# Kernel optimization log

Measured on AMD Instinct MI355X. Metric: run time of the kernel, lower is better.

The kernel has to match this reference:

```python
import jax, jax.numpy as jnp
import numpy as np

N = 2048            # num nodes
AVG_DEG = 16
E0 = N * AVG_DEG    # random edges; self-loops appended -> E = E0 + N
IN_FEATS = 256
H = 16              # num_heads
HS = 32             # hidden_size (forced by linear001 = Linear(32,16))
D = HS // H         # head_dim = 2
EPS = 1e-5


def gat_conv(x, src, dst, W, al, ar, b):
    # DGL-style GATConv: x [N,F] -> [N,H,D]
    feat = (x @ W).reshape(N, H, D)                      # [N,H,D]
    el = (feat * al[None]).sum(-1)                       # [N,H] (src term)
    er = (feat * ar[None]).sum(-1)                       # [N,H] (dst term)
    e = jax.nn.leaky_relu(el[src] + er[dst], 0.2)        # [E,H]
    m = jax.ops.segment_max(e, dst, num_segments=N)      # segment softmax over incoming edges
    ex = jnp.exp(e - m[dst])
    s = jax.ops.segment_sum(ex, dst, num_segments=N)
    alpha = ex / s[dst]                                  # [E,H]
    out = jax.ops.segment_sum(alpha[:, :, None] * feat[src], dst, num_segments=N)
    return out + b.reshape(1, H, D)


def setup_inputs() -> dict:
    key = jax.random.key(0)
    ks = jax.random.split(key, 40)
    rn = lambda k, s, sc=0.1: (jax.random.normal(k, s, jnp.float32) * sc)
    loops = jnp.arange(N, dtype=jnp.int32)
    src = jnp.concatenate([jax.random.randint(ks[0], (E0,), 0, N, jnp.int32), loops])
    dst = jnp.concatenate([jax.random.randint(ks[1], (E0,), 0, N, jnp.int32), loops])
    inp = {
        'features': jax.random.normal(ks[2], (N, IN_FEATS), jnp.float32),
        'src': src, 'dst': dst,
        # GATConv 1
        'W1': rn(ks[3], (IN_FEATS, HS)), 'al1': rn(ks[4], (H, D)), 'ar1': rn(ks[5], (H, D)), 'bg1': rn(ks[6], (HS,)),
        # GATConv 2
        'W2': rn(ks[7], (HS, HS)), 'al2': rn(ks[8], (H, D)), 'ar2': rn(ks[9], (H, D)), 'bg2': rn(ks[10], (HS,)),
        # dense MHA projections
        'qw': rn(ks[11], (HS, HS)), 'qb': rn(ks[12], (HS,)),
        'kw': rn(ks[13], (HS, HS)), 'kb': rn(ks[14], (HS,)),
        'vw': rn(ks[15], (HS, HS)), 'vb': rn(ks[16], (HS,)),
        'ow': rn(ks[17], (HS, HS)), 'ob': rn(ks[18], (HS,)),
        # batchnorm affine
        'bn_g': jnp.ones((HS,), jnp.float32), 'bn_b': jnp.zeros((HS,), jnp.float32),
        # mlp
        'm1w': rn(ks[19], (HS, HS // 2)), 'm1b': rn(ks[20], (HS // 2,)),
        'm2w': rn(ks[21], (HS // 2, HS)), 'm2b': rn(ks[22], (HS,)),
        # scoring head
        'w001': rn(ks[23], (32, 16)), 'b001': rn(ks[24], (16,)),
        'w01': rn(ks[25], (16, 8)), 'b01': rn(ks[26], (8,)),
        'w1': rn(ks[27], (8, 4)), 'b1': rn(ks[28], (4,)),
        'w2': rn(ks[29], (4, 1)), 'b2': rn(ks[30], (1,)),
    }
    return inp


def reference(features, src, dst, W1, al1, ar1, bg1, W2, al2, ar2, bg2,
              qw, qb, kw, kb, vw, vb, ow, ob, bn_g, bn_b,
              m1w, m1b, m2w, m2b, w001, b001, w01, b01, w1, b1, w2, b2):
    h = gat_conv(features, src, dst, W1, al1, ar1, bg1).reshape(N, HS)
    h = gat_conv(h, src, dst, W2, al2, ar2, bg2).reshape(N, HS)
    # manual dense multi-head attention across all nodes
    Q = (h @ qw + qb).reshape(N, H, D)
    K = (h @ kw + kb).reshape(N, H, D)
    V = (h @ vw + vb).reshape(N, H, D)
    scores = jnp.einsum('nhd,mhd->hnm', Q, K) / jnp.sqrt(jnp.float32(D))  # [H,N,N]
    attn = jax.nn.softmax(scores, axis=-1)
    ao = jnp.einsum('hnm,mhd->nhd', attn, V).reshape(N, HS)
    ao = ao @ ow + ob
    # BatchNorm1d (training mode: batch stats, biased variance)
    mu = ao.mean(0)
    var = ao.var(0)
    ao = (ao - mu) / jnp.sqrt(var + EPS) * bn_g + bn_b
    # MLP
    ao = jax.nn.relu(ao @ m1w + m1b)
    ao = jax.nn.relu(ao @ m2w + m2b)
    # scoring head
    z = jax.nn.leaky_relu(ao @ w001 + b001, 0.01)
    z = jax.nn.leaky_relu(z @ w01 + b01, 0.01)
    z = jax.nn.leaky_relu(z @ w1 + b1, 0.01)
    return jax.nn.sigmoid(z @ w2 + b2)  # [N,1]
```

## Files before the change

### kernel.cpp

```cpp
#include <hip/hip_runtime.h>
#include <math.h>

#define NN 2048
#define NH 16
#define HSZ 32
#define INF_ 256
#define CAP 64

__global__ void __launch_bounds__(256) k_front(
    const float* __restrict__ x, const float* __restrict__ W1,
    const float* __restrict__ al, const float* __restrict__ ar,
    const int* __restrict__ src, const int* __restrict__ dst, int E,
    unsigned int* __restrict__ cnt, int* __restrict__ adj,
    const unsigned int* __restrict__ poisonRef, float* __restrict__ feat,
    float* __restrict__ el, float* __restrict__ er) {
    __shared__ float xs[4][INF_];
    __shared__ float row[4][HSZ];
    const int tid = threadIdx.x;
    const int gtid = blockIdx.x * 256 + tid;
    const int lane = tid & 63, wsl = tid >> 6, gw = gtid >> 6;
    const int j = lane & 31, half = lane >> 5;

    if (gtid < E) {
        unsigned int P = *poisonRef;
        int d = dst[gtid];
        unsigned int old = atomicAdd(&cnt[d], 1u);
        unsigned int pos = old - P;
        if (pos < CAP) adj[d * CAP + pos] = src[gtid];
    }

    int n = gw;
    ((float4*)xs[wsl])[lane] = ((const float4*)(x + (size_t)n * INF_))[lane];
    __syncthreads();
    float acc = 0.f;
    const float4* x4 = (const float4*)xs[wsl];
#pragma unroll
    for (int k4 = 0; k4 < 32; ++k4) {
        float4 xq = x4[half * 32 + k4];
        int k = half * 128 + 4 * k4;
        acc += xq.x * W1[(k + 0) * HSZ + j];
        acc += xq.y * W1[(k + 1) * HSZ + j];
        acc += xq.z * W1[(k + 2) * HSZ + j];
        acc += xq.w * W1[(k + 3) * HSZ + j];
    }
    acc += __shfl_xor(acc, 32);
    if (half == 0) {
        feat[n * HSZ + j] = acc;
        row[wsl][j] = acc;
    }
    __syncthreads();
    if (lane < NH) {
        el[n * NH + lane] =
            row[wsl][2 * lane] * al[2 * lane] + row[wsl][2 * lane + 1] * al[2 * lane + 1];
    } else if (lane < 2 * NH) {
        int h = lane - NH;
        er[n * NH + h] =
            row[wsl][2 * h] * ar[2 * h] + row[wsl][2 * h + 1] * ar[2 * h + 1];
    }
}

__global__ void __launch_bounds__(256) k_seg_gat2(
    const unsigned int* __restrict__ cnt, const int* __restrict__ adj,
    const unsigned int* __restrict__ poisonRef,
    const float* __restrict__ el, const float* __restrict__ er,
    const float* __restrict__ feat, const float* __restrict__ bg,
    const float* __restrict__ W2, const float* __restrict__ al2,
    const float* __restrict__ ar2, float* __restrict__ feat2,
    float* __restrict__ el2, float* __restrict__ er2) {
    __shared__ float row[4][HSZ];
    __shared__ float xv[4][HSZ];
    const int tid = threadIdx.x;
    const int gtid = blockIdx.x * 256 + tid;
    const int lane = tid & 63, wsl = tid >> 6, gw = gtid >> 6;
    const int j = lane & 31, half = lane >> 5;
    int n = gw;
    int h = lane >> 2, q = lane & 3;
    unsigned int deg = cnt[n] - *poisonRef;
    if (deg > CAP) deg = CAP;
    int base = n * CAP;
    float erv = er[n * NH + h];
    float sum = 0.f, a0 = 0.f, a1 = 0.f;
    for (unsigned int jj = q; jj < deg; jj += 4) {
        int s = adj[base + jj];
        float v = el[s * NH + h] + erv;
        v = v > 0.f ? v : 0.2f * v;
        float ex = __expf(v);
        float2 f = ((const float2*)feat)[s * NH + h];
        sum += ex; a0 += ex * f.x; a1 += ex * f.y;
    }
    sum += __shfl_xor(sum, 1); a0 += __shfl_xor(a0, 1); a1 += __shfl_xor(a1, 1);
    sum += __shfl_xor(sum, 2); a0 += __shfl_xor(a0, 2); a1 += __shfl_xor(a1, 2);
    if (q == 0) {
        float rs = 1.f / sum;
        row[wsl][2 * h]     = a0 * rs + bg[2 * h];
        row[wsl][2 * h + 1] = a1 * rs + bg[2 * h + 1];
    }
    __syncthreads();
    float acc = 0.f;
#pragma unroll
    for (int c = half * 16; c < half * 16 + 16; ++c) acc += row[wsl][c] * W2[c * HSZ + j];
    acc += __shfl_xor(acc, 32);
    if (half == 0) {
        feat2[n * HSZ + j] = acc;
        xv[wsl][j] = acc;
    }
    __syncthreads();
    if (lane < NH) {
        el2[n * NH + lane] =
            xv[wsl][2 * lane] * al2[2 * lane] + xv[wsl][2 * lane + 1] * al2[2 * lane + 1];
    } else if (lane < 2 * NH) {
        int h2 = lane - NH;
        er2[n * NH + h2] =
            xv[wsl][2 * h2] * ar2[2 * h2] + xv[wsl][2 * h2 + 1] * ar2[2 * h2 + 1];
    }
}

__global__ void __launch_bounds__(256) k_seg_qkv(
    const unsigned int* __restrict__ cnt, const int* __restrict__ adj,
    const unsigned int* __restrict__ poisonRef,
    const float* __restrict__ el2, const float* __restrict__ er2,
    const float* __restrict__ feat2, const float* __restrict__ bg,
    const float* __restrict__ qw, const float* __restrict__ qb,
    const float* __restrict__ kw, const float* __restrict__ kb,
    const float* __restrict__ vw, const float* __restrict__ vb,
    float* __restrict__ Q, float* __restrict__ KV) {
    __shared__ float row[4][HSZ];
    const int tid = threadIdx.x;
    const int gtid = blockIdx.x * 256 + tid;
    const int lane = tid & 63, wsl = tid >> 6, gw = gtid >> 6;
    const int j = lane & 31, half = lane >> 5;
    int n = gw;
    int h = lane >> 2, q = lane & 3;
    unsigned int deg = cnt[n] - *poisonRef;
    if (deg > CAP) deg = CAP;
    int base = n * CAP;
    float erv = er2[n * NH + h];
    float sum = 0.f, a0 = 0.f, a1 = 0.f;
    for (unsigned int jj = q; jj < deg; jj += 4) {
        int s = adj[base + jj];
        float v = el2[s * NH + h] + erv;
        v = v > 0.f ? v : 0.2f * v;
        float ex = __expf(v);
        float2 f = ((const float2*)feat2)[s * NH + h];
        sum += ex; a0 += ex * f.x; a1 += ex * f.y;
    }
    sum += __shfl_xor(sum, 1); a0 += __shfl_xor(a0, 1); a1 += __shfl_xor(a1, 1);
    sum += __shfl_xor(sum, 2); a0 += __shfl_xor(a0, 2); a1 += __shfl_xor(a1, 2);
    if (q == 0) {
        float rs = 1.f / sum;
        row[wsl][2 * h]     = a0 * rs + bg[2 * h];
        row[wsl][2 * h + 1] = a1 * rs + bg[2 * h + 1];
    }
    __syncthreads();
    float qa = 0.f, ka = 0.f, va = 0.f;
#pragma unroll
    for (int c = half * 16; c < half * 16 + 16; ++c) {
        float hv = row[wsl][c];
        qa += hv * qw[c * HSZ + j];
        ka += hv * kw[c * HSZ + j];
        va += hv * vw[c * HSZ + j];
    }
    qa += __shfl_xor(qa, 32);
    ka += __shfl_xor(ka, 32);
    va += __shfl_xor(va, 32);
    if (half == 0) {
        const float QS = 0.70710678118654752f * 1.44269504088896340f;
        Q[n * HSZ + j] = (qa + qb[j]) * QS;
        int hh = j >> 1, d = j & 1;
        KV[(hh * NN + n) * 4 + d]     = ka + kb[j];
        KV[(hh * NN + n) * 4 + 2 + d] = va + vb[j];
    }
}

__global__ void __launch_bounds__(256) k_attn16(
    const float* __restrict__ Q, const float* __restrict__ KV,
    float* __restrict__ ao, float* __restrict__ bnbuf, int* __restrict__ done) {
    const int gtid = blockIdx.x * 256 + threadIdx.x;
    if (blockIdx.x == 0) {
        if (threadIdx.x < 64) bnbuf[threadIdx.x] = 0.f;
        else if (threadIdx.x == 64) *done = 0;
    }
    const int gw = gtid >> 6;
    const int lane = gtid & 63;
    int hh = gw >> 7;
    int q0 = (gw & 127) * 16;
    const float4* KV4 = (const float4*)KV + hh * NN;
    const float2* Q2 = (const float2*)Q;
    float qx[16], qy[16], sm[16], a0[16], a1[16];
#pragma unroll
    for (int i = 0; i < 16; ++i) {
        float2 qq = Q2[(q0 + i) * NH + hh];
        qx[i] = qq.x; qy[i] = qq.y;
        sm[i] = 0.f; a0[i] = 0.f; a1[i] = 0.f;
    }
#pragma unroll 2
    for (int it = 0; it < NN / 64; ++it) {
        float4 kv = KV4[it * 64 + lane];
#pragma unroll
        for (int i = 0; i < 16; ++i) {
            float pe = exp2f(qx[i] * kv.x + qy[i] * kv.y);
            sm[i] += pe; a0[i] += pe * kv.z; a1[i] += pe * kv.w;
        }
    }
#pragma unroll
    for (int i = 0; i < 16; ++i) {
#pragma unroll
        for (int off = 32; off; off >>= 1) {
            sm[i] += __shfl_xor(sm[i], off);
            a0[i] += __shfl_xor(a0[i], off);
            a1[i] += __shfl_xor(a1[i], off);
        }
        if (lane == 0) {
            float rs = 1.f / sm[i];
            ((float2*)ao)[(q0 + i) * NH + hh] = make_float2(a0[i] * rs, a1[i] * rs);
        }
    }
}

#define M1W 0
#define M2W 512
#define W001 1024
#define W01 1536
#define W1O 1664
#define W2O 1696
#define M1B 1700
#define M2B 1716
#define B001 1748
#define B01 1764
#define B1O 1772
#define B2O 1776
__global__ void __launch_bounds__(256) k_opt(
    const float* __restrict__ ao, const float* __restrict__ ow,
    const float* __restrict__ ob, const float* __restrict__ bn_g,
    const float* __restrict__ bn_b, const float* __restrict__ m1w,
    const float* __restrict__ m1b, const float* __restrict__ m2w,
    const float* __restrict__ m2b, const float* __restrict__ w001,
    const float* __restrict__ b001, const float* __restrict__ w01,
    const float* __restrict__ b01, const float* __restrict__ w1,
    const float* __restrict__ b1, const float* __restrict__ w2,
    const float* __restrict__ b2, float* __restrict__ bnbuf,
    int* __restrict__ done, float* __restrict__ out) {
    __shared__ float w_s[1844];
    __shared__ float ao_s[8][33];
    __shared__ float xr[8][33];
    __shared__ float AB[64];
    __shared__ float yb[8][17];
    __shared__ float zb[8][33];
    __shared__ float ab[8][17];
    __shared__ float bb[8][9];
    __shared__ float cb[8][5];
    const int t = threadIdx.x;
    const int n0 = blockIdx.x * 8;

    w_s[M1W + t] = m1w[t];            w_s[M1W + 256 + t] = m1w[256 + t];
    w_s[M2W + t] = m2w[t];            w_s[M2W + 256 + t] = m2w[256 + t];
    w_s[W001 + t] = w001[t];          w_s[W001 + 256 + t] = w001[256 + t];
    if (t < 128) w_s[W01 + t] = w01[t];
    if (t < 32) { w_s[W1O + t] = w1[t]; w_s[M2B + t] = m2b[t]; }
    if (t < 16) { w_s[M1B + t] = m1b[t]; w_s[B001 + t] = b001[t]; }
    if (t < 8) w_s[B01 + t] = b01[t];
    if (t < 4) { w_s[B1O + t] = b1[t]; w_s[W2O + t] = w2[t]; }
    if (t == 0) w_s[B2O] = b2[0];
    {
        int nl = t >> 5, j = t & 31;
        ao_s[nl][j] = ao[(n0 + nl) * HSZ + j];
    }
    __syncthreads();

    const int nl = t >> 5, j = t & 31;
    {
        float a = ob[j];
#pragma unroll
        for (int c = 0; c < HSZ; ++c) a += ao_s[nl][c] * ow[c * HSZ + j];
        xr[nl][j] = a;
    }
    __syncthreads();
    if (t < HSZ) {
        float s = 0.f, qsum = 0.f;
#pragma unroll
        for (int r = 0; r < 8; ++r) { float v = xr[r][t]; s += v; qsum += v * v; }
        atomicAdd(&bnbuf[t], s);
        atomicAdd(&bnbuf[HSZ + t], qsum);
    }
    __syncthreads();
    if (t == 0) {
        __hip_atomic_fetch_add(done, 1, __ATOMIC_RELAXED, __HIP_MEMORY_SCOPE_AGENT);
        while (__hip_atomic_load(done, __ATOMIC_RELAXED, __HIP_MEMORY_SCOPE_AGENT) < 256)
            __builtin_amdgcn_s_sleep(1);
    }
    __syncthreads();
    if (t < HSZ) {
        const float invN = 1.f / NN;
        float s = __hip_atomic_load(&bnbuf[t], __ATOMIC_RELAXED, __HIP_MEMORY_SCOPE_AGENT);
        float qs = __hip_atomic_load(&bnbuf[HSZ + t], __ATOMIC_RELAXED, __HIP_MEMORY_SCOPE_AGENT);
        float mu = s * invN;
        float var = qs * invN - mu * mu;
        float A = rsqrtf(var + 1e-5f) * bn_g[t];
        AB[t] = A;
        AB[HSZ + t] = bn_b[t] - mu * A;
    }
    __syncthreads();
    xr[nl][j] = xr[nl][j] * AB[j] + AB[HSZ + j];
    __syncthreads();

    const int s5 = j;
    if (s5 < 16) {
        float a = w_s[M1B + s5];
#pragma unroll
        for (int i = 0; i < 32; ++i) a += xr[nl][i] * w_s[M1W + i * 16 + s5];
        yb[nl][s5] = fmaxf(a, 0.f);
    }
    __syncthreads();
    {
        float a = w_s[M2B + s5];
#pragma unroll
        for (int i = 0; i < 16; ++i) a += yb[nl][i] * w_s[M2W + i * 32 + s5];
        zb[nl][s5] = fmaxf(a, 0.f);
    }
    __syncthreads();
    if (s5 < 16) {
        float a = w_s[B001 + s5];
#pragma unroll
        for (int i = 0; i < 32; ++i) a += zb[nl][i] * w_s[W001 + i * 16 + s5];
        ab[nl][s5] = a > 0.f ? a : 0.01f * a;
    }
    __syncthreads();
    if (s5 < 8) {
        float a = w_s[B01 + s5];
#pragma unroll
        for (int i = 0; i < 16; ++i) a += ab[nl][i] * w_s[W01 + i * 8 + s5];
        bb[nl][s5] = a > 0.f ? a : 0.01f * a;
    }
    __syncthreads();
    if (s5 < 4) {
        float a = w_s[B1O + s5];
#pragma unroll
        for (int i = 0; i < 8; ++i) a += bb[nl][i] * w_s[W1O + i * 4 + s5];
        cb[nl][s5] = a > 0.f ? a : 0.01f * a;
    }
    __syncthreads();
    if (s5 == 0) {
        float d = w_s[B2O];
#pragma unroll
        for (int i = 0; i < 4; ++i) d += cb[nl][i] * w_s[W2O + i];
        out[n0 + nl] = 1.f / (1.f + __expf(-d));
    }
}

extern "C" void kernel_launch(void* const* d_in, const int* in_sizes, int n_in,
                              void* d_out, int out_size, void* d_ws, size_t ws_size,
                              hipStream_t stream) {
    const float* features = (const float*)d_in[0];
    const int* src = (const int*)d_in[1];
    const int* dst = (const int*)d_in[2];
    const float* W1 = (const float*)d_in[3];
    const float* al1 = (const float*)d_in[4];
    const float* ar1 = (const float*)d_in[5];
    const float* bg1 = (const float*)d_in[6];
    const float* W2 = (const float*)d_in[7];
    const float* al2 = (const float*)d_in[8];
    const float* ar2 = (const float*)d_in[9];
    const float* bg2 = (const float*)d_in[10];
    const float* qw = (const float*)d_in[11];
    const float* qb = (const float*)d_in[12];
    const float* kw = (const float*)d_in[13];
    const float* kb = (const float*)d_in[14];
    const float* vw = (const float*)d_in[15];
    const float* vb = (const float*)d_in[16];
    const float* ow = (const float*)d_in[17];
    const float* ob = (const float*)d_in[18];
    const float* bn_g = (const float*)d_in[19];
    const float* bn_b = (const float*)d_in[20];
    const float* m1w = (const float*)d_in[21];
    const float* m1b = (const float*)d_in[22];
    const float* m2w = (const float*)d_in[23];
    const float* m2b = (const float*)d_in[24];
    const float* w001 = (const float*)d_in[25];
    const float* b001 = (const float*)d_in[26];
    const float* w01 = (const float*)d_in[27];
    const float* b01 = (const float*)d_in[28];
    const float* w1 = (const float*)d_in[29];
    const float* b1 = (const float*)d_in[30];
    const float* w2 = (const float*)d_in[31];
    const float* b2 = (const float*)d_in[32];

    int E = in_sizes[1];

    float* wsp = (float*)d_ws;
    float* feat = wsp;
    float* el = feat + NN * HSZ;
    float* er = el + NN * NH;
    float* feat2 = er + NN * NH;
    float* el2 = feat2 + NN * HSZ;
    float* er2 = el2 + NN * NH;
    float* Q = er2 + NN * NH;
    float* KV = Q + NN * HSZ;
    float* ao = KV + NN * HSZ * 2;
    float* bnbuf = ao + NN * HSZ;
    int* done = (int*)(bnbuf + 64);
    unsigned int* cnt = (unsigned int*)(done + 16);
    int* adj = (int*)(cnt + NN);
    unsigned int* poisonRef = (unsigned int*)(adj + NN * CAP);

    dim3 b256(256);
    k_front<<<512, b256, 0, stream>>>(features, W1, al1, ar1, src, dst, E,
                                      cnt, adj, poisonRef, feat, el, er);
    k_seg_gat2<<<512, b256, 0, stream>>>(cnt, adj, poisonRef, el, er, feat, bg1,
                                         W2, al2, ar2, feat2, el2, er2);
    k_seg_qkv<<<512, b256, 0, stream>>>(cnt, adj, poisonRef, el2, er2, feat2, bg2,
                                        qw, qb, kw, kb, vw, vb, Q, KV);
    k_attn16<<<512, b256, 0, stream>>>(Q, KV, ao, bnbuf, done);
    k_opt<<<256, b256, 0, stream>>>(ao, ow, ob, bn_g, bn_b, m1w, m1b, m2w, m2b,
                                    w001, b001, w01, b01, w1, b1, w2, b2,
                                    bnbuf, done, (float*)d_out);
}
```

Before: 182.6 us.

## Fuse stage pairs into two persistent kernels joined by grid barriers

Merges the front projection with the first GAT aggregation, and the second aggregation plus QKV with dense attention, into two kernels. Each pair is separated by a software grid barrier: an atomic counter offset by the poison value, spun on with sleep. This removes two kernel launches and their inter-kernel gaps. The barrier relies on all 512 blocks being co-resident (launch bounds of 2 blocks per CU), which risks deadlock if occupancy is insufficient and adds spin cost.

```diff
diff --git a/kernel.cpp b/kernel.cpp
--- a/kernel.cpp
+++ b/kernel.cpp
@@ -6,213 +6,222 @@
 #define HSZ 32
 #define INF_ 256
 #define CAP 64
-
-__global__ void __launch_bounds__(256) k_front(
+#define NBLK 512
+
+__device__ __forceinline__ void gbar(unsigned int* ctr, unsigned int P, unsigned int nb) {
+    __syncthreads();
+    if (threadIdx.x == 0) {
+        __hip_atomic_fetch_add(ctr, 1u, __ATOMIC_RELEASE, __HIP_MEMORY_SCOPE_AGENT);
+        while (__hip_atomic_load(ctr, __ATOMIC_RELAXED, __HIP_MEMORY_SCOPE_AGENT) - P < nb)
+            __builtin_amdgcn_s_sleep(8);
+        (void)__hip_atomic_load(ctr, __ATOMIC_ACQUIRE, __HIP_MEMORY_SCOPE_AGENT);
+    }
+    __syncthreads();
+}
+
+__global__ void __launch_bounds__(256, 2) k_A(
     const float* __restrict__ x, const float* __restrict__ W1,
-    const float* __restrict__ al, const float* __restrict__ ar,
+    const float* __restrict__ al1, const float* __restrict__ ar1,
     const int* __restrict__ src, const int* __restrict__ dst, int E,
     unsigned int* __restrict__ cnt, int* __restrict__ adj,
-    const unsigned int* __restrict__ poisonRef, float* __restrict__ feat,
-    float* __restrict__ el, float* __restrict__ er) {
+    const unsigned int* __restrict__ poisonRef,
+    float* __restrict__ feat, float* __restrict__ el, float* __restrict__ er,
+    const float* __restrict__ bg1, const float* __restrict__ W2,
+    const float* __restrict__ al2, const float* __restrict__ ar2,
+    float* __restrict__ feat2, float* __restrict__ el2, float* __restrict__ er2,
+    unsigned int* __restrict__ bars) {
     __shared__ float xs[4][INF_];
-    __shared__ float row[4][HSZ];
-    const int tid = threadIdx.x;
-    const int gtid = blockIdx.x * 256 + tid;
-    const int lane = tid & 63, wsl = tid >> 6, gw = gtid >> 6;
-    const int j = lane & 31, half = lane >> 5;
-
-    if (gtid < E) {
-        unsigned int P = *poisonRef;
-        int d = dst[gtid];
-        unsigned int old = atomicAdd(&cnt[d], 1u);
-        unsigned int pos = old - P;
-        if (pos < CAP) adj[d * CAP + pos] = src[gtid];
-    }
-
-    int n = gw;
-    ((float4*)xs[wsl])[lane] = ((const float4*)(x + (size_t)n * INF_))[lane];
-    __syncthreads();
-    float acc = 0.f;
-    const float4* x4 = (const float4*)xs[wsl];
-#pragma unroll
-    for (int k4 = 0; k4 < 32; ++k4) {
-        float4 xq = x4[half * 32 + k4];
-        int k = half * 128 + 4 * k4;
-        acc += xq.x * W1[(k + 0) * HSZ + j];
-        acc += xq.y * W1[(k + 1) * HSZ + j];
-        acc += xq.z * W1[(k + 2) * HSZ + j];
-        acc += xq.w * W1[(k + 3) * HSZ + j];
-    }
-    acc += __shfl_xor(acc, 32);
-    if (half == 0) {
-        feat[n * HSZ + j] = acc;
-        row[wsl][j] = acc;
-    }
-    __syncthreads();
-    if (lane < NH) {
-        el[n * NH + lane] =
-            row[wsl][2 * lane] * al[2 * lane] + row[wsl][2 * lane + 1] * al[2 * lane + 1];
-    } else if (lane < 2 * NH) {
-        int h = lane - NH;
-        er[n * NH + h] =
-            row[wsl][2 * h] * ar[2 * h] + row[wsl][2 * h + 1] * ar[2 * h + 1];
-    }
-}
-
-__global__ void __launch_bounds__(256) k_seg_gat2(
-    const unsigned int* __restrict__ cnt, const int* __restrict__ adj,
-    const unsigned int* __restrict__ poisonRef,
-    const float* __restrict__ el, const float* __restrict__ er,
-    const float* __restrict__ feat, const float* __restrict__ bg,
-    const float* __restrict__ W2, const float* __restrict__ al2,
-    const float* __restrict__ ar2, float* __restrict__ feat2,
-    float* __restrict__ el2, float* __restrict__ er2) {
     __shared__ float row[4][HSZ];
     __shared__ float xv[4][HSZ];
     const int tid = threadIdx.x;
     const int gtid = blockIdx.x * 256 + tid;
     const int lane = tid & 63, wsl = tid >> 6, gw = gtid >> 6;
     const int j = lane & 31, half = lane >> 5;
-    int n = gw;
-    int h = lane >> 2, q = lane & 3;
-    unsigned int deg = cnt[n] - *poisonRef;
-    if (deg > CAP) deg = CAP;
-    int base = n * CAP;
-    float erv = er[n * NH + h];
-    float sum = 0.f, a0 = 0.f, a1 = 0.f;
-    for (unsigned int jj = q; jj < deg; jj += 4) {
-        int s = adj[base + jj];
-        float v = el[s * NH + h] + erv;
-        v = v > 0.f ? v : 0.2f * v;
-        float ex = __expf(v);
-        float2 f = ((const float2*)feat)[s * NH + h];
-        sum += ex; a0 += ex * f.x; a1 += ex * f.y;
-    }
-    sum += __shfl_xor(sum, 1); a0 += __shfl_xor(a0, 1); a1 += __shfl_xor(a1, 1);
-    sum += __shfl_xor(sum, 2); a0 += __shfl_xor(a0, 2); a1 += __shfl_xor(a1, 2);
-    if (q == 0) {
-        float rs = 1.f / sum;
-        row[wsl][2 * h]     = a0 * rs + bg[2 * h];
-        row[wsl][2 * h + 1] = a1 * rs + bg[2 * h + 1];
-    }
-    __syncthreads();
-    float acc = 0.f;
-#pragma unroll
-    for (int c = half * 16; c < half * 16 + 16; ++c) acc += row[wsl][c] * W2[c * HSZ + j];
-    acc += __shfl_xor(acc, 32);
-    if (half == 0) {
-        feat2[n * HSZ + j] = acc;
-        xv[wsl][j] = acc;
-    }
-    __syncthreads();
-    if (lane < NH) {
-        el2[n * NH + lane] =
-            xv[wsl][2 * lane] * al2[2 * lane] + xv[wsl][2 * lane + 1] * al2[2 * lane + 1];
-    } else if (lane < 2 * NH) {
-        int h2 = lane - NH;
-        er2[n * NH + h2] =
-            xv[wsl][2 * h2] * ar2[2 * h2] + xv[wsl][2 * h2 + 1] * ar2[2 * h2 + 1];
+    const int n = gw;
+    const unsigned int P = __hip_atomic_load(poisonRef, __ATOMIC_RELAXED, __HIP_MEMORY_SCOPE_AGENT);
+
+    if (gtid < E) {
+        int d = dst[gtid];
+        unsigned int pos = atomicAdd(&cnt[d], 1u) - P;
+        if (pos < CAP) adj[d * CAP + pos] = src[gtid];
+    }
+    ((float4*)xs[wsl])[lane] = ((const float4*)(x + (size_t)n * INF_))[lane];
+    __syncthreads();
+    {
+        float acc = 0.f;
+        const float4* x4 = (const float4*)xs[wsl];
+#pragma unroll
+        for (int k4 = 0; k4 < 32; ++k4) {
+            float4 xq = x4[half * 32 + k4];
+            int k = half * 128 + 4 * k4;
+            acc += xq.x * W1[(k + 0) * HSZ + j];
+            acc += xq.y * W1[(k + 1) * HSZ + j];
+            acc += xq.z * W1[(k + 2) * HSZ + j];
+            acc += xq.w * W1[(k + 3) * HSZ + j];
+        }
+        acc += __shfl_xor(acc, 32);
+        if (half == 0) {
+            feat[n * HSZ + j] = acc;
+            row[wsl][j] = acc;
+        }
+        __syncthreads();
+        if (lane < NH) {
+            el[n * NH + lane] =
+                row[wsl][2 * lane] * al1[2 * lane] + row[wsl][2 * lane + 1] * al1[2 * lane + 1];
+        } else if (lane < 2 * NH) {
+            int h = lane - NH;
+            er[n * NH + h] =
+                row[wsl][2 * h] * ar1[2 * h] + row[wsl][2 * h + 1] * ar1[2 * h + 1];
+        }
+    }
+
+    gbar(&bars[0], P, NBLK);
+
+    {
+        int h = lane >> 2, q = lane & 3;
+        unsigned int deg = cnt[n] - P;
+        if (deg > CAP) deg = CAP;
+        int base = n * CAP;
+        float erv = er[n * NH + h];
+        float sum = 0.f, a0 = 0.f, a1 = 0.f;
+        for (unsigned int jj = q; jj < deg; jj += 4) {
+            int s = adj[base + jj];
+            float v = el[s * NH + h] + erv;
+            v = v > 0.f ? v : 0.2f * v;
+            float ex = __expf(v);
+            float2 f = ((const float2*)feat)[s * NH + h];
+            sum += ex; a0 += ex * f.x; a1 += ex * f.y;
+        }
+        sum += __shfl_xor(sum, 1); a0 += __shfl_xor(a0, 1); a1 += __shfl_xor(a1, 1);
+        sum += __shfl_xor(sum, 2); a0 += __shfl_xor(a0, 2); a1 += __shfl_xor(a1, 2);
+        if (q == 0) {
+            float rs = 1.f / sum;
+            row[wsl][2 * h]     = a0 * rs + bg1[2 * h];
+            row[wsl][2 * h + 1] = a1 * rs + bg1[2 * h + 1];
+        }
+        __syncthreads();
+        float acc = 0.f;
+#pragma unroll
+        for (int c = half * 16; c < half * 16 + 16; ++c) acc += row[wsl][c] * W2[c * HSZ + j];
+        acc += __shfl_xor(acc, 32);
+        if (half == 0) {
+            feat2[n * HSZ + j] = acc;
+            xv[wsl][j] = acc;
+        }
+        __syncthreads();
+        if (lane < NH) {
+            el2[n * NH + lane] =
+                xv[wsl][2 * lane] * al2[2 * lane] + xv[wsl][2 * lane + 1] * al2[2 * lane + 1];
+        } else if (lane < 2 * NH) {
+            int h2 = lane - NH;
+            er2[n * NH + h2] =
+                xv[wsl][2 * h2] * ar2[2 * h2] + xv[wsl][2 * h2 + 1] * ar2[2 * h2 + 1];
+        }
     }
 }
 
-__global__ void __launch_bounds__(256) k_seg_qkv(
+__global__ void __launch_bounds__(256, 2) k_B(
     const unsigned int* __restrict__ cnt, const int* __restrict__ adj,
     const unsigned int* __restrict__ poisonRef,
     const float* __restrict__ el2, const float* __restrict__ er2,
-    const float* __restrict__ feat2, const float* __restrict__ bg,
+    const float* __restrict__ feat2, const float* __restrict__ bg2,
     const float* __restrict__ qw, const float* __restrict__ qb,
     const float* __restrict__ kw, const float* __restrict__ kb,
     const float* __restrict__ vw, const float* __restrict__ vb,
-    float* __restrict__ Q, float* __restrict__ KV) {
+    float* __restrict__ Q, float* __restrict__ KV, float* __restrict__ ao,
+    float* __restrict__ bnbuf, int* __restrict__ done,
+    unsigned int* __restrict__ bars) {
     __shared__ float row[4][HSZ];
     const int tid = threadIdx.x;
     const int gtid = blockIdx.x * 256 + tid;
     const int lane = tid & 63, wsl = tid >> 6, gw = gtid >> 6;
     const int j = lane & 31, half = lane >> 5;
-    int n = gw;
-    int h = lane >> 2, q = lane & 3;
-    unsigned int deg = cnt[n] - *poisonRef;
-    if (deg > CAP) deg = CAP;
-    int base = n * CAP;
-    float erv = er2[n * NH + h];
-    float sum = 0.f, a0 = 0.f, a1 = 0.f;
-    for (unsigned int jj = q; jj < deg; jj += 4) {
-        int s = adj[base + jj];
-        float v = el2[s * NH + h] + erv;
-        v = v > 0.f ? v : 0.2f * v;
-        float ex = __expf(v);
-        float2 f = ((const float2*)feat2)[s * NH + h];
-        sum += ex; a0 += ex * f.x; a1 += ex * f.y;
-    }
-    sum += __shfl_xor(sum, 1); a0 += __shfl_xor(a0, 1); a1 += __shfl_xor(a1, 1);
-    sum += __shfl_xor(sum, 2); a0 += __shfl_xor(a0, 2); a1 += __shfl_xor(a1, 2);
-    if (q == 0) {
-        float rs = 1.f / sum;
-        row[wsl][2 * h]     = a0 * rs + bg[2 * h];
-        row[wsl][2 * h + 1] = a1 * rs + bg[2 * h + 1];
-    }
-    __syncthreads();
-    float qa = 0.f, ka = 0.f, va = 0.f;
-#pragma unroll
-    for (int c = half * 16; c < half * 16 + 16; ++c) {
-        float hv = row[wsl][c];
-        qa += hv * qw[c * HSZ + j];
-        ka += hv * kw[c * HSZ + j];
-        va += hv * vw[c * HSZ + j];
-    }
-    qa += __shfl_xor(qa, 32);
-    ka += __shfl_xor(ka, 32);
-    va += __shfl_xor(va, 32);
-    if (half == 0) {
-        const float QS = 0.70710678118654752f * 1.44269504088896340f;
-        Q[n * HSZ + j] = (qa + qb[j]) * QS;
-        int hh = j >> 1, d = j & 1;
-        KV[(hh * NN + n) * 4 + d]     = ka + kb[j];
-        KV[(hh * NN + n) * 4 + 2 + d] = va + vb[j];
-    }
-}
-
-__global__ void __launch_bounds__(256) k_attn16(
-    const float* __restrict__ Q, const float* __restrict__ KV,
-    float* __restrict__ ao, float* __restrict__ bnbuf, int* __restrict__ done) {
-    const int gtid = blockIdx.x * 256 + threadIdx.x;
+    const unsigned int P = __hip_atomic_load(poisonRef, __ATOMIC_RELAXED, __HIP_MEMORY_SCOPE_AGENT);
+
     if (blockIdx.x == 0) {
-        if (threadIdx.x < 64) bnbuf[threadIdx.x] = 0.f;
-        else if (threadIdx.x == 64) *done = 0;
-    }
-    const int gw = gtid >> 6;
-    const int lane = gtid & 63;
-    int hh = gw >> 7;
-    int q0 = (gw & 127) * 16;
-    const float4* KV4 = (const float4*)KV + hh * NN;
-    const float2* Q2 = (const float2*)Q;
-    float qx[16], qy[16], sm[16], a0[16], a1[16];
-#pragma unroll
-    for (int i = 0; i < 16; ++i) {
-        float2 qq = Q2[(q0 + i) * NH + hh];
-        qx[i] = qq.x; qy[i] = qq.y;
-        sm[i] = 0.f; a0[i] = 0.f; a1[i] = 0.f;
-    }
+        if (tid < 64) bnbuf[tid] = 0.f;
+        else if (tid == 64) *done = 0;
+    }
+
+    {
+        const int n = gw;
+        int h = lane >> 2, q = lane & 3;
+        unsigned int deg = cnt[n] - P;
+        if (deg > CAP) deg = CAP;
+        int base = n * CAP;
+        float erv = er2[n * NH + h];
+        float sum = 0.f, a0 = 0.f, a1 = 0.f;
+        for (unsigned int jj = q; jj < deg; jj += 4) {
+            int s = adj[base + jj];
+            float v = el2[s * NH + h] + erv;
+            v = v > 0.f ? v : 0.2f * v;
+            float ex = __expf(v);
+            float2 f = ((const float2*)feat2)[s * NH + h];
+            sum += ex; a0 += ex * f.x; a1 += ex * f.y;
+        }
+        sum += __shfl_xor(sum, 1); a0 += __shfl_xor(a0, 1); a1 += __shfl_xor(a1, 1);
+        sum += __shfl_xor(sum, 2); a0 += __shfl_xor(a0, 2); a1 += __shfl_xor(a1, 2);
+        if (q == 0) {
+            float rs = 1.f / sum;
+            row[wsl][2 * h]     = a0 * rs + bg2[2 * h];
+            row[wsl][2 * h + 1] = a1 * rs + bg2[2 * h + 1];
+        }
+        __syncthreads();
+        float qa = 0.f, ka = 0.f, va = 0.f;
+#pragma unroll
+        for (int c = half * 16; c < half * 16 + 16; ++c) {
+            float hv = row[wsl][c];
+            qa += hv * qw[c * HSZ + j];
+            ka += hv * kw[c * HSZ + j];
+            va += hv * vw[c * HSZ + j];
+        }
+        qa += __shfl_xor(qa, 32);
+        ka += __shfl_xor(ka, 32);
+        va += __shfl_xor(va, 32);
+        if (half == 0) {
+            const float QS = 0.70710678118654752f * 1.44269504088896340f;
+            Q[n * HSZ + j] = (qa + qb[j]) * QS;
+            int hh = j >> 1, d = j & 1;
+            KV[(hh * NN + n) * 4 + d]     = ka + kb[j];
+            KV[(hh * NN + n) * 4 + 2 + d] = va + vb[j];
+        }
+    }
+
+    gbar(&bars[1], P, NBLK);
+
+    {
+        int hh = gw >> 7;
+        int q0 = (gw & 127) * 16;
+        const float4* KV4 = (const float4*)KV + hh * NN;
+        const float2* Q2 = (const float2*)Q;
+        float qx[16], qy[16], sm[16], a0[16], a1[16];
+#pragma unroll
+        for (int i = 0; i < 16; ++i) {
+            float2 qq = Q2[(q0 + i) * NH + hh];
+            qx[i] = qq.x; qy[i] = qq.y;
+            sm[i] = 0.f; a0[i] = 0.f; a1[i] = 0.f;
+        }
 #pragma unroll 2
-    for (int it = 0; it < NN / 64; ++it) {
-        float4 kv = KV4[it * 64 + lane];
+        for (int it = 0; it < NN / 64; ++it) {
+            float4 kv = KV4[it * 64 + lane];
+#pragma unroll
+            for (int i = 0; i < 16; ++i) {
+                float pe = exp2f(qx[i] * kv.x + qy[i] * kv.y);
+                sm[i] += pe; a0[i] += pe * kv.z; a1[i] += pe * kv.w;
+            }
+        }
 #pragma unroll
         for (int i = 0; i < 16; ++i) {
-            float pe = exp2f(qx[i] * kv.x + qy[i] * kv.y);
-            sm[i] += pe; a0[i] += pe * kv.z; a1[i] += pe * kv.w;
-        }
-    }
-#pragma unroll
-    for (int i = 0; i < 16; ++i) {
-#pragma unroll
-        for (int off = 32; off; off >>= 1) {
-            sm[i] += __shfl_xor(sm[i], off);
-            a0[i] += __shfl_xor(a0[i], off);
-            a1[i] += __shfl_xor(a1[i], off);
-        }
-        if (lane == 0) {
-            float rs = 1.f / sm[i];
-            ((float2*)ao)[(q0 + i) * NH + hh] = make_float2(a0[i] * rs, a1[i] * rs);
+#pragma unroll
+            for (int off = 32; off; off >>= 1) {
+                sm[i] += __shfl_xor(sm[i], off);
+                a0[i] += __shfl_xor(a0[i], off);
+                a1[i] += __shfl_xor(a1[i], off);
+            }
+            if (lane == 0) {
+                float rs = 1.f / sm[i];
+                ((float2*)ao)[(q0 + i) * NH + hh] = make_float2(a0[i] * rs, a1[i] * rs);
+            }
         }
     }
 }
@@ -398,18 +407,18 @@
     float* ao = KV + NN * HSZ * 2;
     float* bnbuf = ao + NN * HSZ;
     int* done = (int*)(bnbuf + 64);
-    unsigned int* cnt = (unsigned int*)(done + 16);
+    unsigned int* bars = (unsigned int*)(done + 16);
+    unsigned int* cnt = bars + 16;
     int* adj = (int*)(cnt + NN);
     unsigned int* poisonRef = (unsigned int*)(adj + NN * CAP);
 
     dim3 b256(256);
-    k_front<<<512, b256, 0, stream>>>(features, W1, al1, ar1, src, dst, E,
-                                      cnt, adj, poisonRef, feat, el, er);
-    k_seg_gat2<<<512, b256, 0, stream>>>(cnt, adj, poisonRef, el, er, feat, bg1,
-                                         W2, al2, ar2, feat2, el2, er2);
-    k_seg_qkv<<<512, b256, 0, stream>>>(cnt, adj, poisonRef, el2, er2, feat2, bg2,
-                                        qw, qb, kw, kb, vw, vb, Q, KV);
-    k_attn16<<<512, b256, 0, stream>>>(Q, KV, ao, bnbuf, done);
+    k_A<<<NBLK, b256, 0, stream>>>(features, W1, al1, ar1, src, dst, E,
+                                   cnt, adj, poisonRef, feat, el, er,
+                                   bg1, W2, al2, ar2, feat2, el2, er2, bars);
+    k_B<<<NBLK, b256, 0, stream>>>(cnt, adj, poisonRef, el2, er2, feat2, bg2,
+                                   qw, qb, kw, kb, vw, vb, Q, KV, ao,
+                                   bnbuf, done, bars);
     k_opt<<<256, b256, 0, stream>>>(ao, ow, ob, bn_g, bn_b, m1w, m1b, m2w, m2b,
                                     w001, b001, w01, b01, w1, b1, w2, b2,
                                     bnbuf, done, (float*)d_out);
```

Result: slower. 253.3 us (+38.7%).
